# Kernel optimization log

Measured on AMD Instinct MI355X. Metric: run time of the kernel, lower is better.

The kernel has to match this reference:

```python
import jax, jax.numpy as jnp
import numpy as np

B, T, C, H, HS = 2, 2048, 1024, 16, 64


def setup_inputs() -> dict:
    key = jax.random.key(0)
    ks = jax.random.split(key, 7)
    x = jax.random.normal(ks[0], (B, T, C), dtype=jnp.float32)
    # causal mask, broadcast over batch (True = attend)
    attention_mask = jnp.broadcast_to(jnp.tril(jnp.ones((T, T), dtype=bool)), (B, T, T))
    s = 1.0 / np.sqrt(C)
    wq = jax.random.normal(ks[1], (H, C, HS), dtype=jnp.float32) * s   # per-head query Linear (no bias)
    wk = jax.random.normal(ks[2], (H, C, HS), dtype=jnp.float32) * s
    wv = jax.random.normal(ks[3], (H, C, HS), dtype=jnp.float32) * s
    wproj = jax.random.normal(ks[4], (H * HS, C), dtype=jnp.float32) * (1.0 / np.sqrt(H * HS))
    bproj = jnp.zeros((C,), dtype=jnp.float32)
    return {"x": x, "attention_mask": attention_mask,
            "wq": wq, "wk": wk, "wv": wv, "wproj": wproj, "bproj": bproj}


def reference(x, attention_mask, wq, wk, wv, wproj, bproj):
    # per-head projections: [B,H,T,HS]
    q = jnp.einsum('btc,hcd->bhtd', x, wq)
    k = jnp.einsum('btc,hcd->bhtd', x, wk)
    v = jnp.einsum('btc,hcd->bhtd', x, wv)
    scale = 1.0 / jnp.sqrt(jnp.asarray(HS, dtype=x.dtype))
    wei = jnp.einsum('bhtd,bhsd->bhts', q, k) * scale          # [B,H,T,T]
    wei = jnp.where(attention_mask[:, None, :, :], wei, -jnp.inf)
    wei = jax.nn.softmax(wei, axis=-1)
    out = jnp.einsum('bhts,bhsd->bhtd', wei, v)                 # [B,H,T,HS]
    out = out.transpose(0, 2, 1, 3).reshape(B, T, H * HS)       # concat heads
    return out @ wproj + bproj                                  # [B,T,C]
```

## Files before the change

### kernel.cpp

```cpp
#include <hip/hip_runtime.h>
#include <math.h>

typedef float f32x4 __attribute__((ext_vector_type(4)));
typedef __bf16 bf16x8 __attribute__((ext_vector_type(8)));
typedef unsigned short u16x8 __attribute__((ext_vector_type(8)));
typedef unsigned short u16x4 __attribute__((ext_vector_type(4)));

#define DEV static __device__ __forceinline__

DEV unsigned short f2bf(float f) {
    unsigned int u = __builtin_bit_cast(unsigned int, f);
    u += 0x7fffu + ((u >> 16) & 1u);
    return (unsigned short)(u >> 16);
}

#define GLD16(gp, lp) __builtin_amdgcn_global_load_lds( \
    (__attribute__((address_space(1))) void*)(gp),      \
    (__attribute__((address_space(3))) void*)(lp), 16, 0, 0)

#define WAITBAR(N) asm volatile("s_waitcnt vmcnt(" #N ")\n\ts_barrier" ::: "memory")
#define BARRIER()  asm volatile("s_barrier" ::: "memory")

__global__ __launch_bounds__(256) void k_prep(const float* __restrict__ x,
                                              const float* __restrict__ wq,
                                              const float* __restrict__ wk,
                                              const float* __restrict__ wv,
                                              const float* __restrict__ wproj,
                                              unsigned short* __restrict__ xb,
                                              unsigned short* __restrict__ WqkvT,
                                              unsigned short* __restrict__ WprojT) {
    const int bid = blockIdx.x, tid = threadIdx.x;
    if (bid < 2048) {
        int i = bid * 256 + tid;
        const float4* p = (const float4*)(x + (size_t)i * 8);
        float4 a = p[0], b = p[1];
        u16x8 o;
        o[0] = f2bf(a.x); o[1] = f2bf(a.y); o[2] = f2bf(a.z); o[3] = f2bf(a.w);
        o[4] = f2bf(b.x); o[5] = f2bf(b.y); o[6] = f2bf(b.z); o[7] = f2bf(b.w);
        *(u16x8*)(xb + (size_t)i * 8) = o;
        return;
    }
    __shared__ unsigned short t[64][68];
    if (bid < 2816) {
        int zb = bid - 2048;
        int z = zb >> 4, wsel = z >> 4, zz = z & 15;
        const float* src = (wsel == 0 ? wq : wsel == 1 ? wk : wv) + (size_t)zz * 65536;
        int r0 = (zb & 15) * 64;
#pragma unroll
        for (int it = 0; it < 4; ++it) {
            int r = (tid >> 4) + it * 16;
            int c4 = (tid & 15) * 4;
            float4 v = *(const float4*)&src[(size_t)(r0 + r) * 64 + c4];
            t[c4 + 0][r] = f2bf(v.x);
            t[c4 + 1][r] = f2bf(v.y);
            t[c4 + 2][r] = f2bf(v.z);
            t[c4 + 3][r] = f2bf(v.w);
        }
        __syncthreads();
#pragma unroll
        for (int it = 0; it < 4; ++it) {
            int c = (tid >> 4) + it * 16;
            int r4 = (tid & 15) * 4;
            u16x4 o;
            o[0] = t[c][r4 + 0]; o[1] = t[c][r4 + 1];
            o[2] = t[c][r4 + 2]; o[3] = t[c][r4 + 3];
            int row = wsel * 1024 + zz * 64 + c;
            *(u16x4*)&WqkvT[(size_t)row * 1024 + r0 + r4] = o;
        }
    } else {
        int zb = bid - 2816;
        int r0 = (zb & 15) * 64, c0 = (zb >> 4) * 64;
#pragma unroll
        for (int it = 0; it < 4; ++it) {
            int r = (tid >> 4) + it * 16;
            int c4 = (tid & 15) * 4;
            float4 v = *(const float4*)&wproj[(size_t)(r0 + r) * 1024 + c0 + c4];
            t[c4 + 0][r] = f2bf(v.x);
            t[c4 + 1][r] = f2bf(v.y);
            t[c4 + 2][r] = f2bf(v.z);
            t[c4 + 3][r] = f2bf(v.w);
        }
        __syncthreads();
#pragma unroll
        for (int it = 0; it < 4; ++it) {
            int c = (tid >> 4) + it * 16;
            int r4 = (tid & 15) * 4;
            u16x4 o;
            o[0] = t[c][r4 + 0]; o[1] = t[c][r4 + 1];
            o[2] = t[c][r4 + 2]; o[3] = t[c][r4 + 3];
            *(u16x4*)&WprojT[(size_t)(c0 + c) * 1024 + r0 + r4] = o;
        }
    }
}

template <int STAGE, int NB, int SUPM, int SUPN>
__global__ __launch_bounds__(256) void k_gemm(const unsigned short* __restrict__ A,
                                              const unsigned short* __restrict__ Bt,
                                              int Kd,
                                              float* __restrict__ outF,
                                              const float* __restrict__ bias,
                                              unsigned short* __restrict__ Qb,
                                              unsigned short* __restrict__ Kb,
                                              unsigned short* __restrict__ Vt) {
    __shared__ unsigned short As[2][128 * 64] __attribute__((aligned(16)));
    __shared__ unsigned short Bs[2][128 * 64] __attribute__((aligned(16)));
    const int tid = threadIdx.x, l = tid & 63, w = tid >> 6;
    constexpr int BN_CH = NB / SUPN;
    const int orig = blockIdx.x;
    const int xcd = orig & 7, sdx = orig >> 3;
    const int bm = (xcd / BN_CH) * SUPM + (sdx % SUPM);
    const int bn = (xcd % BN_CH) * SUPN + (sdx / SUPM);
    const int wr = w >> 1, wc = w & 1;
    const int g = l >> 4, q = l & 15;
    f32x4 acc[4][4] = {};
    const unsigned short* gA = A + (size_t)(bm * 128 + w * 8 + (l >> 3)) * Kd + (l & 7) * 8;
    const unsigned short* gB = Bt + (size_t)(bn * 128 + w * 8 + (l >> 3)) * Kd + (l & 7) * 8;

#define GSTAGE(buf, k0) do {                                                  \
        _Pragma("unroll")                                                     \
        for (int it = 0; it < 4; ++it) {                                      \
            GLD16(gA + (size_t)(it * 32) * Kd + (k0), &As[buf][(it * 32 + w * 8) * 64]); \
            GLD16(gB + (size_t)(it * 32) * Kd + (k0), &Bs[buf][(it * 32 + w * 8) * 64]); \
        }                                                                     \
    } while (0)

    const int nt = Kd >> 6;
    GSTAGE(0, 0);
    int cur = 0;
    for (int t = 0; t < nt; ++t) {
        if (t + 1 < nt) {
            GSTAGE(cur ^ 1, (t + 1) << 6);
            WAITBAR(8);
        } else {
            WAITBAR(0);
        }
#pragma unroll
        for (int ks = 0; ks < 2; ++ks) {
            bf16x8 af[4], bfr[4];
#pragma unroll
            for (int mi = 0; mi < 4; ++mi)
                af[mi] = *(const bf16x8*)&As[cur][(wr * 64 + mi * 16 + q) * 64 + ks * 32 + g * 8];
#pragma unroll
            for (int ni = 0; ni < 4; ++ni)
                bfr[ni] = *(const bf16x8*)&Bs[cur][(wc * 64 + ni * 16 + q) * 64 + ks * 32 + g * 8];
#pragma unroll
            for (int mi = 0; mi < 4; ++mi)
#pragma unroll
                for (int ni = 0; ni < 4; ++ni)
                    acc[mi][ni] = __builtin_amdgcn_mfma_f32_16x16x32_bf16(
                        af[mi], bfr[ni], acc[mi][ni], 0, 0, 0);
        }
        BARRIER();
        cur ^= 1;
    }
#undef GSTAGE
#pragma unroll
    for (int mi = 0; mi < 4; ++mi)
#pragma unroll
        for (int ni = 0; ni < 4; ++ni)
#pragma unroll
            for (int r = 0; r < 4; ++r) {
                float c = acc[mi][ni][r];
                int m = bm * 128 + wr * 64 + mi * 16 + g * 4 + r;
                int n = bn * 128 + wc * 64 + ni * 16 + q;
                if (STAGE == 1) {
                    int b = m >> 11, t = m & 2047;
                    int proj = n >> 10, rr = n & 1023, h = rr >> 6, d = rr & 63;
                    int bh = b * 16 + h;
                    if (proj == 0)
                        Qb[((size_t)bh * 2048 + t) * 64 + d] = f2bf(c * 0.18033688011112042f);
                    else if (proj == 1)
                        Kb[((size_t)bh * 2048 + t) * 64 + d] = f2bf(c);
                    else
                        Vt[((size_t)bh * 64 + d) * 2048 + t] = f2bf(c);
                } else {
                    outF[(size_t)m * 1024 + n] = c + bias[n];
                }
            }
}

__global__ __launch_bounds__(256) void k_attn(const unsigned short* __restrict__ Qb,
                                              const unsigned short* __restrict__ Kb,
                                              const unsigned short* __restrict__ Vt,
                                              unsigned short* __restrict__ att) {
    __shared__ unsigned short Ks[2][2][4096] __attribute__((aligned(16)));
    __shared__ unsigned short Vs[2][2][4096] __attribute__((aligned(16)));
    __shared__ unsigned short P[4][16][72];
    const int tid = threadIdx.x, l = tid & 63, w = tid >> 6;
    const int pj = blockIdx.x, bh = blockIdx.y;
    const int b = bh >> 4, h = bh & 15;
    const int ql = l & 15, g = l >> 4;
    const unsigned short* Qp = Qb + (size_t)bh * 2048 * 64;
    const unsigned short* Kp = Kb + (size_t)bh * 2048 * 64;
    const unsigned short* Vp = Vt + (size_t)bh * 64 * 2048;

    const int sr0 = w * 16 + (l >> 3);
    const int sch = (l & 7) ^ (l >> 3);
    const unsigned short* gK0 = Kp + (size_t)sr0 * 64 + sch * 8;
    const unsigned short* gK1 = gK0 + 8 * 64;
    const unsigned short* gV0 = Vp + (size_t)sr0 * 2048 + sch * 8;
    const unsigned short* gV1 = gV0 + 8 * 2048;

#define ATT_STAGE(buf, kvb) do {                                                  \
        GLD16(gK0 + (size_t)(kvb) * 64, &Ks[buf][0][(w * 16) * 64]);              \
        GLD16(gK1 + (size_t)(kvb) * 64, &Ks[buf][0][(w * 16 + 8) * 64]);          \
        GLD16(gK0 + (size_t)((kvb) + 64) * 64, &Ks[buf][1][(w * 16) * 64]);       \
        GLD16(gK1 + (size_t)((kvb) + 64) * 64, &Ks[buf][1][(w * 16 + 8) * 64]);   \
        GLD16(gV0 + (kvb), &Vs[buf][0][(w * 16) * 64]);                           \
        GLD16(gV1 + (kvb), &Vs[buf][0][(w * 16 + 8) * 64]);                       \
        GLD16(gV0 + (kvb) + 64, &Vs[buf][1][(w * 16) * 64]);                      \
        GLD16(gV1 + (kvb) + 64, &Vs[buf][1][(w * 16 + 8) * 64]);                  \
    } while (0)

    for (int ph = 0; ph < 2; ++ph) {
        const int qt = ph ? (31 - pj) : pj;
        const int qg = qt * 64 + w * 16 + ql;
        const int minqg = qt * 64 + w * 16;
        const int nkv2 = (qt + 2) >> 1;

        bf16x8 qf0 = *(const bf16x8*)(Qp + (size_t)qg * 64 + g * 8);
        bf16x8 qf1 = *(const bf16x8*)(Qp + (size_t)qg * 64 + 32 + g * 8);
        f32x4 ot[4] = {};
        float mrun = -1e30f, lsum = 0.f;

        ATT_STAGE(0, 0);
        int cur = 0;

        for (int kb = 0; kb < nkv2; ++kb) {
            if (kb + 1 < nkv2) {
                ATT_STAGE(cur ^ 1, (kb + 1) * 128);
                WAITBAR(8);
            } else {
                WAITBAR(0);
            }
#pragma unroll
            for (int sub = 0; sub < 2; ++sub) {
                const int kvb = kb * 128 + sub * 64;
                const unsigned short* Kt = &Ks[cur][sub][0];
                const unsigned short* Vtl = &Vs[cur][sub][0];
                f32x4 st[4] = {};
                bf16x8 kf0[4], kf1[4];
#pragma unroll
                for (int f = 0; f < 4; ++f) {
                    int rk = f * 16 + ql, sw = rk & 7;
                    kf0[f] = *(const bf16x8*)&Kt[rk * 64 + ((g ^ sw) * 8)];
                    kf1[f] = *(const bf16x8*)&Kt[rk * 64 + (((g + 4) ^ sw) * 8)];
                }
                __builtin_amdgcn_s_setprio(1);
#pragma unroll
                for (int f = 0; f < 4; ++f) {
                    st[f] = __builtin_amdgcn_mfma_f32_16x16x32_bf16(kf0[f], qf0, st[f], 0, 0, 0);
                    st[f] = __builtin_amdgcn_mfma_f32_16x16x32_bf16(kf1[f], qf1, st[f], 0, 0, 0);
                }
                __builtin_amdgcn_s_setprio(0);
                if (kvb + 63 > minqg) {
#pragma unroll
                    for (int f = 0; f < 4; ++f)
#pragma unroll
                        for (int r = 0; r < 4; ++r)
                            if (kvb + f * 16 + g * 4 + r > qg) st[f][r] = -1e30f;
                }
                float pmax = -1e30f;
#pragma unroll
                for (int f = 0; f < 4; ++f)
#pragma unroll
                    for (int r = 0; r < 4; ++r) pmax = fmaxf(pmax, st[f][r]);
                if (!__all(pmax <= mrun + 8.f)) {
                    float pm = fmaxf(pmax, __shfl_xor(pmax, 16));
                    pm = fmaxf(pm, __shfl_xor(pm, 32));
                    float mnew = fmaxf(mrun, pm);
                    float corr = __builtin_amdgcn_exp2f(mrun - mnew);
                    lsum *= corr;
#pragma unroll
                    for (int f = 0; f < 4; ++f) ot[f] *= corr;
                    mrun = mnew;
                }
                float psum = 0.f;
#pragma unroll
                for (int f = 0; f < 4; ++f) {
                    u16x4 pk;
#pragma unroll
                    for (int r = 0; r < 4; ++r) {
                        float p = __builtin_amdgcn_exp2f(st[f][r] - mrun);
                        psum += p;
                        pk[r] = f2bf(p);
                    }
                    *(u16x4*)&P[w][ql][f * 16 + g * 4] = pk;
                }
                lsum += psum;
                asm volatile("s_waitcnt lgkmcnt(0)" ::: "memory");
#pragma unroll
                for (int dc = 0; dc < 2; ++dc) {
                    bf16x8 pf = *(const bf16x8*)&P[w][ql][dc * 32 + g * 8];
                    __builtin_amdgcn_s_setprio(1);
#pragma unroll
                    for (int f = 0; f < 4; ++f) {
                        int rv = f * 16 + ql, sw = rv & 7;
                        bf16x8 vf = *(const bf16x8*)&Vtl[rv * 64 + (((dc * 4 + g) ^ sw) * 8)];
                        ot[f] = __builtin_amdgcn_mfma_f32_16x16x32_bf16(vf, pf, ot[f], 0, 0, 0);
                    }
                    __builtin_amdgcn_s_setprio(0);
                }
            }
            BARRIER();
            cur ^= 1;
        }
        lsum += __shfl_xor(lsum, 16);
        lsum += __shfl_xor(lsum, 32);
        float inv = 1.f / lsum;
        unsigned short* ap = att + ((size_t)(b * 2048 + qg)) * 1024 + h * 64;
#pragma unroll
        for (int f = 0; f < 4; ++f) {
            u16x4 o;
#pragma unroll
            for (int r = 0; r < 4; ++r) o[r] = f2bf(ot[f][r] * inv);
            *(u16x4*)&ap[f * 16 + g * 4] = o;
        }
    }
#undef ATT_STAGE
}

extern "C" void kernel_launch(void* const* d_in, const int* in_sizes, int n_in,
                              void* d_out, int out_size, void* d_ws, size_t ws_size,
                              hipStream_t stream) {
    const float* x = (const float*)d_in[0];
    const float* wq = (const float*)d_in[2];
    const float* wk = (const float*)d_in[3];
    const float* wv = (const float*)d_in[4];
    const float* wproj = (const float*)d_in[5];
    const float* bproj = (const float*)d_in[6];
    float* out = (float*)d_out;

    char* ws = (char*)d_ws;
    unsigned short* xb     = (unsigned short*)(ws);
    unsigned short* WqkvT  = (unsigned short*)(ws + (8u << 20));
    unsigned short* WprojT = (unsigned short*)(ws + (14u << 20));
    unsigned short* Qb     = (unsigned short*)(ws + (16u << 20));
    unsigned short* Kb     = (unsigned short*)(ws + (24u << 20));
    unsigned short* Vt     = (unsigned short*)(ws + (32u << 20));
    unsigned short* att    = xb;

    k_prep<<<3072, 256, 0, stream>>>(x, wq, wk, wv, wproj, xb, WqkvT, WprojT);
    k_gemm<1, 24, 8, 12><<<768, 256, 0, stream>>>(xb, WqkvT, 1024, nullptr, nullptr, Qb, Kb, Vt);
    k_attn<<<dim3(16, 32), 256, 0, stream>>>(Qb, Kb, Vt, att);
    k_gemm<3, 8, 8, 4><<<256, 256, 0, stream>>>(att, WprojT, 1024, out, bproj, nullptr, nullptr, nullptr);
}
```

Before: 137.0 us.

## Load V fragments directly from global in attention and halve output GEMM tile height

The attention kernel stops staging V tiles through shared memory and instead has each wave load its V fragments straight from global memory into registers on every sub-block. This cuts the LDS footprint and the global-to-LDS traffic, at the cost of uncoalesced, latency-exposed global reads inside the inner loop. Separately, the GEMM gains an M_REP template parameter, and the output projection now uses 64-row tiles with 512 blocks to fill more compute units.

```diff
diff --git a/kernel.cpp b/kernel.cpp
--- a/kernel.cpp
+++ b/kernel.cpp
@@ -93,7 +93,7 @@
     }
 }
 
-template <int STAGE, int NB, int SUPM, int SUPN>
+template <int STAGE, int M_REP, int NB, int SUPM, int SUPN>
 __global__ __launch_bounds__(256) void k_gemm(const unsigned short* __restrict__ A,
                                               const unsigned short* __restrict__ Bt,
                                               int Kd,
@@ -102,7 +102,8 @@
                                               unsigned short* __restrict__ Qb,
                                               unsigned short* __restrict__ Kb,
                                               unsigned short* __restrict__ Vt) {
-    __shared__ unsigned short As[2][128 * 64] __attribute__((aligned(16)));
+    constexpr int BM = M_REP * 32;
+    __shared__ unsigned short As[2][BM * 64] __attribute__((aligned(16)));
     __shared__ unsigned short Bs[2][128 * 64] __attribute__((aligned(16)));
     const int tid = threadIdx.x, l = tid & 63, w = tid >> 6;
     constexpr int BN_CH = NB / SUPN;
@@ -112,16 +113,17 @@
     const int bn = (xcd % BN_CH) * SUPN + (sdx / SUPM);
     const int wr = w >> 1, wc = w & 1;
     const int g = l >> 4, q = l & 15;
-    f32x4 acc[4][4] = {};
-    const unsigned short* gA = A + (size_t)(bm * 128 + w * 8 + (l >> 3)) * Kd + (l & 7) * 8;
+    f32x4 acc[M_REP][4] = {};
+    const unsigned short* gA = A + (size_t)(bm * BM + w * 8 + (l >> 3)) * Kd + (l & 7) * 8;
     const unsigned short* gB = Bt + (size_t)(bn * 128 + w * 8 + (l >> 3)) * Kd + (l & 7) * 8;
 
 #define GSTAGE(buf, k0) do {                                                  \
         _Pragma("unroll")                                                     \
-        for (int it = 0; it < 4; ++it) {                                      \
+        for (int it = 0; it < M_REP; ++it)                                    \
             GLD16(gA + (size_t)(it * 32) * Kd + (k0), &As[buf][(it * 32 + w * 8) * 64]); \
+        _Pragma("unroll")                                                     \
+        for (int it = 0; it < 4; ++it)                                        \
             GLD16(gB + (size_t)(it * 32) * Kd + (k0), &Bs[buf][(it * 32 + w * 8) * 64]); \
-        }                                                                     \
     } while (0)
 
     const int nt = Kd >> 6;
@@ -130,21 +132,21 @@
     for (int t = 0; t < nt; ++t) {
         if (t + 1 < nt) {
             GSTAGE(cur ^ 1, (t + 1) << 6);
-            WAITBAR(8);
+            if constexpr (M_REP == 4) WAITBAR(8); else WAITBAR(6);
         } else {
             WAITBAR(0);
         }
 #pragma unroll
         for (int ks = 0; ks < 2; ++ks) {
-            bf16x8 af[4], bfr[4];
-#pragma unroll
-            for (int mi = 0; mi < 4; ++mi)
-                af[mi] = *(const bf16x8*)&As[cur][(wr * 64 + mi * 16 + q) * 64 + ks * 32 + g * 8];
+            bf16x8 af[M_REP], bfr[4];
+#pragma unroll
+            for (int mi = 0; mi < M_REP; ++mi)
+                af[mi] = *(const bf16x8*)&As[cur][(wr * (M_REP * 16) + mi * 16 + q) * 64 + ks * 32 + g * 8];
 #pragma unroll
             for (int ni = 0; ni < 4; ++ni)
                 bfr[ni] = *(const bf16x8*)&Bs[cur][(wc * 64 + ni * 16 + q) * 64 + ks * 32 + g * 8];
 #pragma unroll
-            for (int mi = 0; mi < 4; ++mi)
+            for (int mi = 0; mi < M_REP; ++mi)
 #pragma unroll
                 for (int ni = 0; ni < 4; ++ni)
                     acc[mi][ni] = __builtin_amdgcn_mfma_f32_16x16x32_bf16(
@@ -155,13 +157,13 @@
     }
 #undef GSTAGE
 #pragma unroll
-    for (int mi = 0; mi < 4; ++mi)
+    for (int mi = 0; mi < M_REP; ++mi)
 #pragma unroll
         for (int ni = 0; ni < 4; ++ni)
 #pragma unroll
             for (int r = 0; r < 4; ++r) {
                 float c = acc[mi][ni][r];
-                int m = bm * 128 + wr * 64 + mi * 16 + g * 4 + r;
+                int m = bm * BM + wr * (M_REP * 16) + mi * 16 + g * 4 + r;
                 int n = bn * 128 + wc * 64 + ni * 16 + q;
                 if (STAGE == 1) {
                     int b = m >> 11, t = m & 2047;
@@ -184,7 +186,6 @@
                                               const unsigned short* __restrict__ Vt,
                                               unsigned short* __restrict__ att) {
     __shared__ unsigned short Ks[2][2][4096] __attribute__((aligned(16)));
-    __shared__ unsigned short Vs[2][2][4096] __attribute__((aligned(16)));
     __shared__ unsigned short P[4][16][72];
     const int tid = threadIdx.x, l = tid & 63, w = tid >> 6;
     const int pj = blockIdx.x, bh = blockIdx.y;
@@ -198,18 +199,12 @@
     const int sch = (l & 7) ^ (l >> 3);
     const unsigned short* gK0 = Kp + (size_t)sr0 * 64 + sch * 8;
     const unsigned short* gK1 = gK0 + 8 * 64;
-    const unsigned short* gV0 = Vp + (size_t)sr0 * 2048 + sch * 8;
-    const unsigned short* gV1 = gV0 + 8 * 2048;
 
 #define ATT_STAGE(buf, kvb) do {                                                  \
         GLD16(gK0 + (size_t)(kvb) * 64, &Ks[buf][0][(w * 16) * 64]);              \
         GLD16(gK1 + (size_t)(kvb) * 64, &Ks[buf][0][(w * 16 + 8) * 64]);          \
         GLD16(gK0 + (size_t)((kvb) + 64) * 64, &Ks[buf][1][(w * 16) * 64]);       \
         GLD16(gK1 + (size_t)((kvb) + 64) * 64, &Ks[buf][1][(w * 16 + 8) * 64]);   \
-        GLD16(gV0 + (kvb), &Vs[buf][0][(w * 16) * 64]);                           \
-        GLD16(gV1 + (kvb), &Vs[buf][0][(w * 16 + 8) * 64]);                       \
-        GLD16(gV0 + (kvb) + 64, &Vs[buf][1][(w * 16) * 64]);                      \
-        GLD16(gV1 + (kvb) + 64, &Vs[buf][1][(w * 16 + 8) * 64]);                  \
     } while (0)
 
     for (int ph = 0; ph < 2; ++ph) {
@@ -229,7 +224,7 @@
         for (int kb = 0; kb < nkv2; ++kb) {
             if (kb + 1 < nkv2) {
                 ATT_STAGE(cur ^ 1, (kb + 1) * 128);
-                WAITBAR(8);
+                WAITBAR(4);
             } else {
                 WAITBAR(0);
             }
@@ -237,7 +232,13 @@
             for (int sub = 0; sub < 2; ++sub) {
                 const int kvb = kb * 128 + sub * 64;
                 const unsigned short* Kt = &Ks[cur][sub][0];
-                const unsigned short* Vtl = &Vs[cur][sub][0];
+                bf16x8 vfr[2][4];
+#pragma unroll
+                for (int dc = 0; dc < 2; ++dc)
+#pragma unroll
+                    for (int f = 0; f < 4; ++f)
+                        vfr[dc][f] = *(const bf16x8*)(Vp + (size_t)(f * 16 + ql) * 2048 +
+                                                      kvb + dc * 32 + g * 8);
                 f32x4 st[4] = {};
                 bf16x8 kf0[4], kf1[4];
 #pragma unroll
@@ -294,11 +295,8 @@
                     bf16x8 pf = *(const bf16x8*)&P[w][ql][dc * 32 + g * 8];
                     __builtin_amdgcn_s_setprio(1);
 #pragma unroll
-                    for (int f = 0; f < 4; ++f) {
-                        int rv = f * 16 + ql, sw = rv & 7;
-                        bf16x8 vf = *(const bf16x8*)&Vtl[rv * 64 + (((dc * 4 + g) ^ sw) * 8)];
-                        ot[f] = __builtin_amdgcn_mfma_f32_16x16x32_bf16(vf, pf, ot[f], 0, 0, 0);
-                    }
+                    for (int f = 0; f < 4; ++f)
+                        ot[f] = __builtin_amdgcn_mfma_f32_16x16x32_bf16(vfr[dc][f], pf, ot[f], 0, 0, 0);
                     __builtin_amdgcn_s_setprio(0);
                 }
             }
@@ -341,7 +339,7 @@
     unsigned short* att    = xb;
 
     k_prep<<<3072, 256, 0, stream>>>(x, wq, wk, wv, wproj, xb, WqkvT, WprojT);
-    k_gemm<1, 24, 8, 12><<<768, 256, 0, stream>>>(xb, WqkvT, 1024, nullptr, nullptr, Qb, Kb, Vt);
+    k_gemm<1, 4, 24, 8, 12><<<768, 256, 0, stream>>>(xb, WqkvT, 1024, nullptr, nullptr, Qb, Kb, Vt);
     k_attn<<<dim3(16, 32), 256, 0, stream>>>(Qb, Kb, Vt, att);
-    k_gemm<3, 8, 8, 4><<<256, 256, 0, stream>>>(att, WprojT, 1024, out, bproj, nullptr, nullptr, nullptr);
-}
+    k_gemm<3, 2, 8, 16, 4><<<512, 256, 0, stream>>>(att, WprojT, 1024, out, bproj, nullptr, nullptr, nullptr);
+}
```

After: 157.7 us. 15.1% more time.
